# Kernel optimization log

Hardware: AMD Instinct MI355X
Metric: run time of the kernel (lower is better)

## Reference

```python
import jax, jax.numpy as jnp
import numpy as np

NH, NL, NP, GA = 8, 4, 4, 8  # num_heads, num_levels, num_points, grid_align_num
SHAPES = np.array([[128, 128], [64, 64], [32, 32], [16, 16]], dtype=np.int64)  # (W, H) per level


def _grid_sample(img, grid):
    """F.grid_sample bilinear, padding_mode='zeros', align_corners=False.
    img: [N,C,H,W], grid: [N,Hg,Wg,2] in [-1,1] (x,y). Returns [N,C,Hg,Wg]."""
    N, C, H, W = img.shape
    x = (grid[..., 0] + 1.0) * (W * 0.5) - 0.5
    y = (grid[..., 1] + 1.0) * (H * 0.5) - 0.5
    x0 = jnp.floor(x)
    y0 = jnp.floor(y)
    wx = (x - x0)[:, None]  # [N,1,Hg,Wg]
    wy = (y - y0)[:, None]
    x0i = x0.astype(jnp.int32)
    y0i = y0.astype(jnp.int32)
    img_flat = img.reshape(N, C, H * W)
    Hg, Wg = grid.shape[1], grid.shape[2]

    def tap(ix, iy):
        valid = (ix >= 0) & (ix < W) & (iy >= 0) & (iy < H)
        lin = jnp.clip(iy, 0, H - 1) * W + jnp.clip(ix, 0, W - 1)
        v = jnp.take_along_axis(img_flat, lin.reshape(N, 1, Hg * Wg), axis=2)
        return v.reshape(N, C, Hg, Wg) * valid[:, None].astype(img.dtype)

    v00 = tap(x0i, y0i)
    v01 = tap(x0i + 1, y0i)
    v10 = tap(x0i, y0i + 1)
    v11 = tap(x0i + 1, y0i + 1)
    return (v00 * (1 - wx) * (1 - wy) + v01 * wx * (1 - wy)
            + v10 * (1 - wx) * wy + v11 * wx * wy)


def setup_inputs() -> dict:
    key = jax.random.key(0)
    ks = jax.random.split(key, 6)
    bs, nq, E = 2, 16384, 256
    total = int((SHAPES[:, 0] * SHAPES[:, 1]).sum())  # 21760
    query = jax.random.normal(ks[0], (bs, nq, E), jnp.float32)
    value = jax.random.normal(ks[1], (bs, total, NH, E // NH), jnp.float32)
    reference_points = jax.random.uniform(ks[2], (bs, nq, 1, NL * 2), jnp.float32)
    W_off = jax.random.normal(ks[3], (NH * NL * NP * 2, E), jnp.float32) * 0.01
    # structured offset bias per init_weights (directional rays, radius ~ point index)
    thetas = jnp.arange(NH, dtype=jnp.float32) * (2.0 * np.pi / NH)
    gi = jnp.stack([jnp.cos(thetas), jnp.sin(thetas)], -1)  # [NH,2]
    gi = gi / jnp.max(jnp.abs(gi), axis=-1, keepdims=True)
    gi = jnp.tile(gi[:, None, None, :], (1, NL, NP, 1))
    gi = gi * jnp.arange(1, NP + 1, dtype=jnp.float32)[None, None, :, None]
    b_off = gi.reshape(-1)
    W_attn = jax.random.normal(ks[4], (NH * NL * NP, E), jnp.float32) * 0.01
    b_attn = jax.random.normal(ks[5], (NH * NL * NP,), jnp.float32) * 0.01
    return {"query": query, "value": value, "reference_points": reference_points,
            "W_off": W_off, "b_off": b_off, "W_attn": W_attn, "b_attn": b_attn,
            "spatial_shapes": np.asarray(SHAPES)}


def reference(query, value, reference_points, W_off, b_off, W_attn, b_attn, spatial_shapes):
    bs, nq, E = query.shape
    d = E // NH
    shapes = np.asarray(spatial_shapes)  # static [L,2] (W,H)

    # sampling offsets and locations (non-deploy path)
    off = (query @ W_off.T + b_off).reshape(bs, nq, NH, NL * NP * 2)
    ref = jnp.tile(reference_points, (1, 1, NH, NP)).reshape(bs, nq, NH, NL * NP * 2)
    # offset_normalizer: (1/spatial_shapes).repeat(1, NP).flatten() -> layout (l, p, xy)
    norm = jnp.asarray(np.tile(1.0 / shapes.astype(np.float32), (1, NP)).reshape(-1))
    loc = (ref + off * norm) * 2.0 - 1.0  # [bs, nq, NH, NL*NP*2]

    # attention weights: softmax over levels*points, regrouped to (L, G, P) layout
    attn = jax.nn.softmax((query @ W_attn.T + b_attn).reshape(bs, nq, NH, NL * NP), axis=-1)
    attn = (attn.reshape(bs, nq // GA, GA, NH, NL, NP)
            .transpose(0, 3, 1, 4, 2, 5)
            .reshape(bs * NH, 1, nq // GA, NL * GA * NP))

    grids = loc.reshape(bs, nq, NH, NL, NP, 2)
    outs = []
    start = 0
    for lvl in range(NL):
        W_, H_ = int(shapes[lvl, 0]), int(shapes[lvl, 1])
        n = H_ * W_
        v = value[:, start:start + n].transpose(0, 2, 3, 1).reshape(bs * NH, d, H_, W_)
        start += n
        g = grids[:, :, :, lvl].transpose(0, 2, 1, 3, 4).reshape(bs * NH, nq // GA, GA * NP, 2)
        outs.append(_grid_sample(v, g))  # [bs*NH, d, nq//GA, GA*NP]
    samp = jnp.concatenate(outs, axis=-1) * attn  # [bs*NH, d, nq//GA, NL*GA*NP]
    # reduce_sum linear with fixed 0/1 weight == sum over levels and points per group slot
    out = samp.reshape(bs * NH, d, nq // GA, NL, GA, NP).sum(axis=(3, 5))
    return out.reshape(bs, NH * d, nq)
```

## Files before the change

kernel.cpp:

```cpp
#include <hip/hip_runtime.h>
#include <hip/hip_bf16.h>


typedef __attribute__((ext_vector_type(4))) float    float4v;
typedef __attribute__((ext_vector_type(8))) _Float16 half8;
typedef __attribute__((ext_vector_type(4))) _Float16 half4;
typedef __attribute__((ext_vector_type(2))) _Float16 half2v;

#define NQ    16384
#define NTOK  21760
#define LREC  48

#define GEMM_BLOCKS 768
#define CONV_BLOCKS 10880

union H8 { half8 v; half2v p[4]; };

#define LDSTR 88
__global__ __launch_bounds__(256) void fused_kernel(
    const float* __restrict__ qf,
    const float* __restrict__ Woff, const float* __restrict__ Wattn,
    const float* __restrict__ boff, const float* __restrict__ battn,
    const float* __restrict__ val,
    _Float16* __restrict__ lh, _Float16* __restrict__ vh) {
  const int tid = threadIdx.x;

  if (blockIdx.x >= GEMM_BLOCKS) {
    int i = (blockIdx.x - GEMM_BLOCKS) * 256 + tid;
    float4v v = ((const float4v*)val)[i];
    half4 o;
    o[0] = (_Float16)v[0]; o[1] = (_Float16)v[1];
    o[2] = (_Float16)v[2]; o[3] = (_Float16)v[3];
    ((half4*)vh)[i] = o;
    return;
  }

  __shared__ _Float16 As[128 * LDSTR];
  __shared__ _Float16 Bs[128 * LDSTR];

  const int lane = tid & 63;
  const int wv   = tid >> 6;
  const int wm   = wv >> 1, wn = wv & 1;
  const int quad = lane >> 4;
  const int r    = lane & 15;
  const int blockM = (blockIdx.x & 255) * 128;
  const int n0     = (blockIdx.x >> 8) * 128;

  float4v acc[4][4];
#pragma unroll
  for (int i = 0; i < 4; ++i)
#pragma unroll
    for (int j = 0; j < 4; ++j) acc[i][j] = (float4v){0.f, 0.f, 0.f, 0.f};

  for (int kc = 0; kc < 4; ++kc) {
    const int k0 = kc * 64;
    if (kc) __syncthreads();
#pragma unroll
    for (int it = 0; it < 8; ++it) {
      int idx = it * 256 + tid;
      int row = idx >> 4, k4 = idx & 15;
      float4v v = *(const float4v*)(qf + (size_t)(blockM + row) * 256 + k0 + k4 * 4);
      half4 o;
      o[0] = (_Float16)v[0]; o[1] = (_Float16)v[1];
      o[2] = (_Float16)v[2]; o[3] = (_Float16)v[3];
      *(half4*)&As[row * LDSTR + k4 * 4] = o;
    }
#pragma unroll
    for (int it = 0; it < 8; ++it) {
      int idx = it * 256 + tid;
      int row = idx >> 4, k4 = idx & 15;
      int n = n0 + row;
      const float* src = (n < 256) ? (Woff + (size_t)n * 256)
                                   : (Wattn + (size_t)(n - 256) * 256);
      float4v v = *(const float4v*)(src + k0 + k4 * 4);
      half4 o;
      o[0] = (_Float16)v[0]; o[1] = (_Float16)v[1];
      o[2] = (_Float16)v[2]; o[3] = (_Float16)v[3];
      *(half4*)&Bs[row * LDSTR + k4 * 4] = o;
    }
    __syncthreads();

#pragma unroll
    for (int kf = 0; kf < 2; ++kf) {
      const int ko = kf * 32 + quad * 8;
      half8 af[4], bf[4];
#pragma unroll
      for (int mi = 0; mi < 4; ++mi)
        af[mi] = *(const half8*)&As[(wm * 64 + mi * 16 + r) * LDSTR + ko];
#pragma unroll
      for (int ni = 0; ni < 4; ++ni)
        bf[ni] = *(const half8*)&Bs[(wn * 64 + ni * 16 + r) * LDSTR + ko];
#pragma unroll
      for (int mi = 0; mi < 4; ++mi)
#pragma unroll
        for (int ni = 0; ni < 4; ++ni)
          acc[mi][ni] = __builtin_amdgcn_mfma_f32_16x16x32_f16(af[mi], bf[ni], acc[mi][ni], 0, 0, 0);
    }
  }

#pragma unroll
  for (int mi = 0; mi < 4; ++mi) {
    const int mb = blockM + wm * 64 + mi * 16 + quad * 4;
#pragma unroll
    for (int ni = 0; ni < 4; ++ni) {
      const int n = n0 + wn * 64 + ni * 16 + r;
      const float bias = (n < 256) ? boff[n] : battn[n - 256];
      const int h    = (n < 256) ? (n >> 5) : ((n - 256) >> 4);
      const int slot = (n < 256) ? (n & 31) : (32 + ((n - 256) & 15));
#pragma unroll
      for (int reg = 0; reg < 4; ++reg) {
        const int bq = mb + reg;
        const int b = bq >> 14, q = bq & 16383;
        lh[((size_t)(b * 8 + h) * NQ + q) * LREC + slot] =
            (_Float16)(acc[mi][ni][reg] + bias);
      }
    }
  }
}

__global__ __launch_bounds__(256) void sample_kernel(
    const _Float16* __restrict__ vh, const float* __restrict__ refp,
    const _Float16* __restrict__ lh, float* __restrict__ out) {
  const int bid   = blockIdx.x;
  const int xcd   = bid & 7;
  const int local = bid >> 3;
  const int hb    = xcd * 2 + (local >> 8);
  const int qt    = local & 255;
  const int h     = hb & 7;
  const int b     = hb >> 3;
  const int tid = threadIdx.x;
  const int c4 = tid & 3;
  const int qi = tid >> 2;
  const int q  = qt * 64 + qi;
  const size_t bq = (size_t)b * NQ + q;
  const _Float16* rec = lh + ((size_t)hb * NQ + q) * LREC;

  float offf[32];
#pragma unroll
  for (int i = 0; i < 4; ++i) {
    half8 oh = *(const half8*)(rec + i * 8);
#pragma unroll
    for (int j = 0; j < 8; ++j) offf[i * 8 + j] = (float)oh[j];
  }
  float al[16];
#pragma unroll
  for (int i = 0; i < 2; ++i) {
    half8 ah = *(const half8*)(rec + 32 + i * 8);
#pragma unroll
    for (int j = 0; j < 8; ++j) al[i * 8 + j] = (float)ah[j];
  }
  float mx = -1e30f;
#pragma unroll
  for (int i = 0; i < 16; ++i) mx = fmaxf(mx, al[i]);
  float ssum = 0.f;
#pragma unroll
  for (int i = 0; i < 16; ++i) {
    float e = __expf(al[i] - mx);
    al[i] = e;
    ssum += e;
  }
  const float inv = 1.0f / ssum;

  float4v rp0 = *(const float4v*)(refp + bq * 8);
  float4v rp1 = *(const float4v*)(refp + bq * 8 + 4);
  const float rpx[4] = {rp0[0], rp0[2], rp1[0], rp1[2]};
  const float rpy[4] = {rp0[1], rp0[3], rp1[1], rp1[3]};

  const _Float16* vb = vh + (size_t)b * NTOK * 256 + h * 32 + c4 * 8;
  float4v acc0 = (float4v){0.f, 0.f, 0.f, 0.f};
  float4v acc1 = (float4v){0.f, 0.f, 0.f, 0.f};

  const int base[4] = {0, 16384, 20480, 21504};

#pragma unroll
  for (int l = 0; l < 4; ++l) {
    const int   W  = 128 >> l;
    const float fW = (float)W;
    const _Float16* vlev = vb + (size_t)base[l] * 256;
    half2v accl[4];
#pragma unroll
    for (int j = 0; j < 4; ++j) accl[j] = (half2v){(_Float16)0, (_Float16)0};
#pragma unroll
    for (int p = 0; p < 4; ++p) {
      const float a  = al[l * 4 + p] * inv;
      const float ox = offf[l * 8 + p * 2];
      const float oy = offf[l * 8 + p * 2 + 1];
      const float x = rpx[p] * fW + ox - 0.5f;
      const float y = rpy[p] * fW + oy - 0.5f;
      const float xf = floorf(x), yf = floorf(y);
      const float fx = x - xf, fy = y - yf;
      const int ix = (int)xf, iy = (int)yf;
      const int ix0 = min(max(ix, 0), W - 1);
      const int ix1 = min(max(ix + 1, 0), W - 1);
      const int iy0 = min(max(iy, 0), W - 1);
      const int iy1 = min(max(iy + 1, 0), W - 1);
      const float wx0 = ((unsigned)ix       < (unsigned)W) ? 1.f - fx : 0.f;
      const float wx1 = ((unsigned)(ix + 1) < (unsigned)W) ? fx       : 0.f;
      const float wy0 = ((unsigned)iy       < (unsigned)W) ? 1.f - fy : 0.f;
      const float wy1 = ((unsigned)(iy + 1) < (unsigned)W) ? fy       : 0.f;
      const _Float16 w00 = (_Float16)(a * wx0 * wy0);
      const _Float16 w01 = (_Float16)(a * wx1 * wy0);
      const _Float16 w10 = (_Float16)(a * wx0 * wy1);
      const _Float16 w11 = (_Float16)(a * wx1 * wy1);
      const half2v h00 = (half2v){w00, w00};
      const half2v h01 = (half2v){w01, w01};
      const half2v h10 = (half2v){w10, w10};
      const half2v h11 = (half2v){w11, w11};
      const _Float16* r0 = vlev + (size_t)(iy0 * W) * 256;
      const _Float16* r1 = vlev + (size_t)(iy1 * W) * 256;
      H8 t00, t01, t10, t11;
      t00.v = *(const half8*)(r0 + ix0 * 256);
      t01.v = *(const half8*)(r0 + ix1 * 256);
      t10.v = *(const half8*)(r1 + ix0 * 256);
      t11.v = *(const half8*)(r1 + ix1 * 256);
#pragma unroll
      for (int j = 0; j < 4; ++j) {
        accl[j] += h00 * t00.p[j] + h01 * t01.p[j]
                 + h10 * t10.p[j] + h11 * t11.p[j];
      }
    }
    acc0[0] += (float)accl[0][0]; acc0[1] += (float)accl[0][1];
    acc0[2] += (float)accl[1][0]; acc0[3] += (float)accl[1][1];
    acc1[0] += (float)accl[2][0]; acc1[1] += (float)accl[2][1];
    acc1[2] += (float)accl[3][0]; acc1[3] += (float)accl[3][1];
  }

  __shared__ float sm[32][65];
#pragma unroll
  for (int j = 0; j < 4; ++j) {
    sm[c4 * 8 + j][qi]     = acc0[j];
    sm[c4 * 8 + 4 + j][qi] = acc1[j];
  }
  __syncthreads();
  const size_t obase = ((size_t)b * 256 + h * 32) * NQ + qt * 64;
#pragma unroll
  for (int i = 0; i < 8; ++i) {
    const int idx = i * 256 + tid;
    const int c = idx >> 6, qq = idx & 63;
    out[obase + (size_t)c * NQ + qq] = sm[c][qq];
  }
}

extern "C" void kernel_launch(void* const* d_in, const int* in_sizes, int n_in,
                              void* d_out, int out_size, void* d_ws, size_t ws_size,
                              hipStream_t stream) {
  const float* query = (const float*)d_in[0];
  const float* value = (const float*)d_in[1];
  const float* refp  = (const float*)d_in[2];
  const float* Woff  = (const float*)d_in[3];
  const float* boff  = (const float*)d_in[4];
  const float* Wattn = (const float*)d_in[5];
  const float* battn = (const float*)d_in[6];
  float* out = (float*)d_out;

  char* ws = (char*)d_ws;
  _Float16* vh = (_Float16*)ws;
  _Float16* lh = (_Float16*)(ws + 22282240);

  fused_kernel<<<GEMM_BLOCKS + CONV_BLOCKS, 256, 0, stream>>>(
      query, Woff, Wattn, boff, battn, value, lh, vh);
  sample_kernel<<<4096, 256, 0, stream>>>(vh, refp, lh, out);
}
```

Baseline: 221.7 us.

## Assign one query per thread with all 32 channels in sample kernel

Reworks the sampling kernel so each thread handles one query across all 32 head channels instead of four threads sharing a query with 8 channels each. Offsets, softmax and bilinear weights are computed once per query rather than replicated four times, and the corner gathers become four contiguous 64-byte reads per thread. In exchange, each thread carries far more registers (32 fp32 accumulators, 16 half2 accumulators, 16 half8 loads), which may cut occupancy, and the block size and grid are halved.

```diff
diff --git a/kernel.cpp b/kernel.cpp
--- a/kernel.cpp
+++ b/kernel.cpp
@@ -118,30 +118,25 @@
   }
 }
 
-__global__ __launch_bounds__(256) void sample_kernel(
+__global__ __launch_bounds__(128) void sample_kernel(
     const _Float16* __restrict__ vh, const float* __restrict__ refp,
     const _Float16* __restrict__ lh, float* __restrict__ out) {
   const int bid   = blockIdx.x;
   const int xcd   = bid & 7;
   const int local = bid >> 3;
-  const int hb    = xcd * 2 + (local >> 8);
-  const int qt    = local & 255;
+  const int hb    = xcd * 2 + (local >> 7);
+  const int qt    = local & 127;
   const int h     = hb & 7;
   const int b     = hb >> 3;
-  const int tid = threadIdx.x;
-  const int c4 = tid & 3;
-  const int qi = tid >> 2;
-  const int q  = qt * 64 + qi;
+  const int tid   = threadIdx.x;
+  const int q     = qt * 128 + tid;
   const size_t bq = (size_t)b * NQ + q;
   const _Float16* rec = lh + ((size_t)hb * NQ + q) * LREC;
 
-  float offf[32];
-#pragma unroll
-  for (int i = 0; i < 4; ++i) {
-    half8 oh = *(const half8*)(rec + i * 8);
-#pragma unroll
-    for (int j = 0; j < 8; ++j) offf[i * 8 + j] = (float)oh[j];
-  }
+  half8 oh[4];
+#pragma unroll
+  for (int i = 0; i < 4; ++i) oh[i] = *(const half8*)(rec + i * 8);
+
   float al[16];
 #pragma unroll
   for (int i = 0; i < 2; ++i) {
@@ -160,15 +155,19 @@
     ssum += e;
   }
   const float inv = 1.0f / ssum;
+#pragma unroll
+  for (int i = 0; i < 16; ++i) al[i] *= inv;
 
   float4v rp0 = *(const float4v*)(refp + bq * 8);
   float4v rp1 = *(const float4v*)(refp + bq * 8 + 4);
   const float rpx[4] = {rp0[0], rp0[2], rp1[0], rp1[2]};
   const float rpy[4] = {rp0[1], rp0[3], rp1[1], rp1[3]};
 
-  const _Float16* vb = vh + (size_t)b * NTOK * 256 + h * 32 + c4 * 8;
-  float4v acc0 = (float4v){0.f, 0.f, 0.f, 0.f};
-  float4v acc1 = (float4v){0.f, 0.f, 0.f, 0.f};
+  const _Float16* vb = vh + (size_t)b * NTOK * 256 + h * 32;
+
+  float accf[32];
+#pragma unroll
+  for (int i = 0; i < 32; ++i) accf[i] = 0.f;
 
   const int base[4] = {0, 16384, 20480, 21504};
 
@@ -177,14 +176,14 @@
     const int   W  = 128 >> l;
     const float fW = (float)W;
     const _Float16* vlev = vb + (size_t)base[l] * 256;
-    half2v accl[4];
-#pragma unroll
-    for (int j = 0; j < 4; ++j) accl[j] = (half2v){(_Float16)0, (_Float16)0};
+    half2v accl[16];
+#pragma unroll
+    for (int j = 0; j < 16; ++j) accl[j] = (half2v){(_Float16)0, (_Float16)0};
 #pragma unroll
     for (int p = 0; p < 4; ++p) {
-      const float a  = al[l * 4 + p] * inv;
-      const float ox = offf[l * 8 + p * 2];
-      const float oy = offf[l * 8 + p * 2 + 1];
+      const float a  = al[l * 4 + p];
+      const float ox = (float)oh[l][p * 2];
+      const float oy = (float)oh[l][p * 2 + 1];
       const float x = rpx[p] * fW + ox - 0.5f;
       const float y = rpy[p] * fW + oy - 0.5f;
       const float xf = floorf(x), yf = floorf(y);
@@ -206,37 +205,43 @@
       const half2v h01 = (half2v){w01, w01};
       const half2v h10 = (half2v){w10, w10};
       const half2v h11 = (half2v){w11, w11};
-      const _Float16* r0 = vlev + (size_t)(iy0 * W) * 256;
-      const _Float16* r1 = vlev + (size_t)(iy1 * W) * 256;
-      H8 t00, t01, t10, t11;
-      t00.v = *(const half8*)(r0 + ix0 * 256);
-      t01.v = *(const half8*)(r0 + ix1 * 256);
-      t10.v = *(const half8*)(r1 + ix0 * 256);
-      t11.v = *(const half8*)(r1 + ix1 * 256);
+      const _Float16* p00 = vlev + (size_t)(iy0 * W + ix0) * 256;
+      const _Float16* p01 = vlev + (size_t)(iy0 * W + ix1) * 256;
+      const _Float16* p10 = vlev + (size_t)(iy1 * W + ix0) * 256;
+      const _Float16* p11 = vlev + (size_t)(iy1 * W + ix1) * 256;
+      H8 t00[4], t01[4], t10[4], t11[4];
 #pragma unroll
       for (int j = 0; j < 4; ++j) {
-        accl[j] += h00 * t00.p[j] + h01 * t01.p[j]
-                 + h10 * t10.p[j] + h11 * t11.p[j];
+        t00[j].v = *(const half8*)(p00 + j * 8);
+        t01[j].v = *(const half8*)(p01 + j * 8);
+        t10[j].v = *(const half8*)(p10 + j * 8);
+        t11[j].v = *(const half8*)(p11 + j * 8);
       }
-    }
-    acc0[0] += (float)accl[0][0]; acc0[1] += (float)accl[0][1];
-    acc0[2] += (float)accl[1][0]; acc0[3] += (float)accl[1][1];
-    acc1[0] += (float)accl[2][0]; acc1[1] += (float)accl[2][1];
-    acc1[2] += (float)accl[3][0]; acc1[3] += (float)accl[3][1];
-  }
-
-  __shared__ float sm[32][65];
-#pragma unroll
-  for (int j = 0; j < 4; ++j) {
-    sm[c4 * 8 + j][qi]     = acc0[j];
-    sm[c4 * 8 + 4 + j][qi] = acc1[j];
-  }
+#pragma unroll
+      for (int j = 0; j < 4; ++j)
+#pragma unroll
+        for (int k = 0; k < 4; ++k)
+          accl[j * 4 + k] += h00 * t00[j].p[k] + h01 * t01[j].p[k]
+                           + h10 * t10[j].p[k] + h11 * t11[j].p[k];
+    }
+#pragma unroll
+    for (int j = 0; j < 4; ++j)
+#pragma unroll
+      for (int k = 0; k < 4; ++k) {
+        accf[j * 8 + k * 2]     += (float)accl[j * 4 + k][0];
+        accf[j * 8 + k * 2 + 1] += (float)accl[j * 4 + k][1];
+      }
+  }
+
+  __shared__ float sm[32][129];
+#pragma unroll
+  for (int c = 0; c < 32; ++c) sm[c][tid] = accf[c];
   __syncthreads();
-  const size_t obase = ((size_t)b * 256 + h * 32) * NQ + qt * 64;
-#pragma unroll
-  for (int i = 0; i < 8; ++i) {
-    const int idx = i * 256 + tid;
-    const int c = idx >> 6, qq = idx & 63;
+  const size_t obase = ((size_t)b * 256 + h * 32) * NQ + qt * 128;
+#pragma unroll
+  for (int i = 0; i < 32; ++i) {
+    const int idx = i * 128 + tid;
+    const int c = idx >> 7, qq = idx & 127;
     out[obase + (size_t)c * NQ + qq] = sm[c][qq];
   }
 }
@@ -259,5 +264,5 @@
 
   fused_kernel<<<GEMM_BLOCKS + CONV_BLOCKS, 256, 0, stream>>>(
       query, Woff, Wattn, boff, battn, value, lh, vh);
-  sample_kernel<<<4096, 256, 0, stream>>>(vh, refp, lh, out);
+  sample_kernel<<<2048, 128, 0, stream>>>(vh, refp, lh, out);
 }
```

Measured after the change: 370.5 us. +67.1%, slower.

## Split sampling across levels per thread and reduce level partials in shared memory

Applied to the files above, without the earlier changes.

Each thread in the sample kernel now handles a single feature level instead of looping over all four, so a block covers 16 queries instead of 64 and the grid grows fourfold. Per-level partial sums go to shared memory and are summed across levels before the coalesced store. The aim is more parallelism and memory-level concurrency for the latency-bound gather loads, plus fewer registers per thread. In exchange, the softmax max and sum and the reference-point loads are repeated by each of the four level threads, and there is extra shared-memory traffic.

```diff
diff --git a/kernel.cpp b/kernel.cpp
--- a/kernel.cpp
+++ b/kernel.cpp
@@ -124,24 +124,19 @@
   const int bid   = blockIdx.x;
   const int xcd   = bid & 7;
   const int local = bid >> 3;
-  const int hb    = xcd * 2 + (local >> 8);
-  const int qt    = local & 255;
+  const int hb    = xcd * 2 + (local >> 10);
+  const int qt    = local & 1023;
   const int h     = hb & 7;
   const int b     = hb >> 3;
   const int tid = threadIdx.x;
   const int c4 = tid & 3;
-  const int qi = tid >> 2;
-  const int q  = qt * 64 + qi;
+  const int l  = (tid >> 2) & 3;
+  const int qi = tid >> 4;
+  const int q  = qt * 16 + qi;
   const size_t bq = (size_t)b * NQ + q;
   const _Float16* rec = lh + ((size_t)hb * NQ + q) * LREC;
 
-  float offf[32];
-#pragma unroll
-  for (int i = 0; i < 4; ++i) {
-    half8 oh = *(const half8*)(rec + i * 8);
-#pragma unroll
-    for (int j = 0; j < 8; ++j) offf[i * 8 + j] = (float)oh[j];
-  }
+  const half8 oh = *(const half8*)(rec + l * 8);
   float al[16];
 #pragma unroll
   for (int i = 0; i < 2; ++i) {
@@ -149,16 +144,14 @@
 #pragma unroll
     for (int j = 0; j < 8; ++j) al[i * 8 + j] = (float)ah[j];
   }
+  const half4 ownl = *(const half4*)(rec + 32 + l * 4);
+
   float mx = -1e30f;
 #pragma unroll
   for (int i = 0; i < 16; ++i) mx = fmaxf(mx, al[i]);
   float ssum = 0.f;
 #pragma unroll
-  for (int i = 0; i < 16; ++i) {
-    float e = __expf(al[i] - mx);
-    al[i] = e;
-    ssum += e;
-  }
+  for (int i = 0; i < 16; ++i) ssum += __expf(al[i] - mx);
   const float inv = 1.0f / ssum;
 
   float4v rp0 = *(const float4v*)(refp + bq * 8);
@@ -166,78 +159,77 @@
   const float rpx[4] = {rp0[0], rp0[2], rp1[0], rp1[2]};
   const float rpy[4] = {rp0[1], rp0[3], rp1[1], rp1[3]};
 
-  const _Float16* vb = vh + (size_t)b * NTOK * 256 + h * 32 + c4 * 8;
-  float4v acc0 = (float4v){0.f, 0.f, 0.f, 0.f};
-  float4v acc1 = (float4v){0.f, 0.f, 0.f, 0.f};
-
-  const int base[4] = {0, 16384, 20480, 21504};
-
-#pragma unroll
-  for (int l = 0; l < 4; ++l) {
-    const int   W  = 128 >> l;
-    const float fW = (float)W;
-    const _Float16* vlev = vb + (size_t)base[l] * 256;
-    half2v accl[4];
-#pragma unroll
-    for (int j = 0; j < 4; ++j) accl[j] = (half2v){(_Float16)0, (_Float16)0};
-#pragma unroll
-    for (int p = 0; p < 4; ++p) {
-      const float a  = al[l * 4 + p] * inv;
-      const float ox = offf[l * 8 + p * 2];
-      const float oy = offf[l * 8 + p * 2 + 1];
-      const float x = rpx[p] * fW + ox - 0.5f;
-      const float y = rpy[p] * fW + oy - 0.5f;
-      const float xf = floorf(x), yf = floorf(y);
-      const float fx = x - xf, fy = y - yf;
-      const int ix = (int)xf, iy = (int)yf;
-      const int ix0 = min(max(ix, 0), W - 1);
-      const int ix1 = min(max(ix + 1, 0), W - 1);
-      const int iy0 = min(max(iy, 0), W - 1);
-      const int iy1 = min(max(iy + 1, 0), W - 1);
-      const float wx0 = ((unsigned)ix       < (unsigned)W) ? 1.f - fx : 0.f;
-      const float wx1 = ((unsigned)(ix + 1) < (unsigned)W) ? fx       : 0.f;
-      const float wy0 = ((unsigned)iy       < (unsigned)W) ? 1.f - fy : 0.f;
-      const float wy1 = ((unsigned)(iy + 1) < (unsigned)W) ? fy       : 0.f;
-      const _Float16 w00 = (_Float16)(a * wx0 * wy0);
-      const _Float16 w01 = (_Float16)(a * wx1 * wy0);
-      const _Float16 w10 = (_Float16)(a * wx0 * wy1);
-      const _Float16 w11 = (_Float16)(a * wx1 * wy1);
-      const half2v h00 = (half2v){w00, w00};
-      const half2v h01 = (half2v){w01, w01};
-      const half2v h10 = (half2v){w10, w10};
-      const half2v h11 = (half2v){w11, w11};
-      const _Float16* r0 = vlev + (size_t)(iy0 * W) * 256;
-      const _Float16* r1 = vlev + (size_t)(iy1 * W) * 256;
-      H8 t00, t01, t10, t11;
-      t00.v = *(const half8*)(r0 + ix0 * 256);
-      t01.v = *(const half8*)(r0 + ix1 * 256);
-      t10.v = *(const half8*)(r1 + ix0 * 256);
-      t11.v = *(const half8*)(r1 + ix1 * 256);
-#pragma unroll
-      for (int j = 0; j < 4; ++j) {
-        accl[j] += h00 * t00.p[j] + h01 * t01.p[j]
-                 + h10 * t10.p[j] + h11 * t11.p[j];
-      }
-    }
-    acc0[0] += (float)accl[0][0]; acc0[1] += (float)accl[0][1];
-    acc0[2] += (float)accl[1][0]; acc0[3] += (float)accl[1][1];
-    acc1[0] += (float)accl[2][0]; acc1[1] += (float)accl[2][1];
-    acc1[2] += (float)accl[3][0]; acc1[3] += (float)accl[3][1];
-  }
-
-  __shared__ float sm[32][65];
+  const int   W    = 128 >> l;
+  const float fW   = (float)W;
+  const int   base = (l == 0) ? 0 : (l == 1) ? 16384 : (l == 2) ? 20480 : 21504;
+  const _Float16* vlev = vh + (size_t)b * NTOK * 256 + h * 32 + c4 * 8
+                            + (size_t)base * 256;
+
+  half2v accl0 = (half2v){(_Float16)0, (_Float16)0};
+  half2v accl1 = (half2v){(_Float16)0, (_Float16)0};
+  half2v accl2 = (half2v){(_Float16)0, (_Float16)0};
+  half2v accl3 = (half2v){(_Float16)0, (_Float16)0};
+
+#pragma unroll
+  for (int p = 0; p < 4; ++p) {
+    const float a  = __expf((float)ownl[p] - mx) * inv;
+    const float ox = (float)oh[p * 2];
+    const float oy = (float)oh[p * 2 + 1];
+    const float x = rpx[p] * fW + ox - 0.5f;
+    const float y = rpy[p] * fW + oy - 0.5f;
+    const float xf = floorf(x), yf = floorf(y);
+    const float fx = x - xf, fy = y - yf;
+    const int ix = (int)xf, iy = (int)yf;
+    const int ix0 = min(max(ix, 0), W - 1);
+    const int ix1 = min(max(ix + 1, 0), W - 1);
+    const int iy0 = min(max(iy, 0), W - 1);
+    const int iy1 = min(max(iy + 1, 0), W - 1);
+    const float wx0 = ((unsigned)ix       < (unsigned)W) ? 1.f - fx : 0.f;
+    const float wx1 = ((unsigned)(ix + 1) < (unsigned)W) ? fx       : 0.f;
+    const float wy0 = ((unsigned)iy       < (unsigned)W) ? 1.f - fy : 0.f;
+    const float wy1 = ((unsigned)(iy + 1) < (unsigned)W) ? fy       : 0.f;
+    const _Float16 w00 = (_Float16)(a * wx0 * wy0);
+    const _Float16 w01 = (_Float16)(a * wx1 * wy0);
+    const _Float16 w10 = (_Float16)(a * wx0 * wy1);
+    const _Float16 w11 = (_Float16)(a * wx1 * wy1);
+    const half2v h00 = (half2v){w00, w00};
+    const half2v h01 = (half2v){w01, w01};
+    const half2v h10 = (half2v){w10, w10};
+    const half2v h11 = (half2v){w11, w11};
+    const _Float16* r0 = vlev + (size_t)(iy0 * W) * 256;
+    const _Float16* r1 = vlev + (size_t)(iy1 * W) * 256;
+    H8 t00, t01, t10, t11;
+    t00.v = *(const half8*)(r0 + ix0 * 256);
+    t01.v = *(const half8*)(r0 + ix1 * 256);
+    t10.v = *(const half8*)(r1 + ix0 * 256);
+    t11.v = *(const half8*)(r1 + ix1 * 256);
+    accl0 += h00 * t00.p[0] + h01 * t01.p[0] + h10 * t10.p[0] + h11 * t11.p[0];
+    accl1 += h00 * t00.p[1] + h01 * t01.p[1] + h10 * t10.p[1] + h11 * t11.p[1];
+    accl2 += h00 * t00.p[2] + h01 * t01.p[2] + h10 * t10.p[2] + h11 * t11.p[2];
+    accl3 += h00 * t00.p[3] + h01 * t01.p[3] + h10 * t10.p[3] + h11 * t11.p[3];
+  }
+
+  float acc0[4], acc1[4];
+  acc0[0] = (float)accl0[0]; acc0[1] = (float)accl0[1];
+  acc0[2] = (float)accl1[0]; acc0[3] = (float)accl1[1];
+  acc1[0] = (float)accl2[0]; acc1[1] = (float)accl2[1];
+  acc1[2] = (float)accl3[0]; acc1[3] = (float)accl3[1];
+
+  __shared__ float sm[4][16][33];
 #pragma unroll
   for (int j = 0; j < 4; ++j) {
-    sm[c4 * 8 + j][qi]     = acc0[j];
-    sm[c4 * 8 + 4 + j][qi] = acc1[j];
+    sm[l][qi][c4 * 8 + j]     = acc0[j];
+    sm[l][qi][c4 * 8 + 4 + j] = acc1[j];
   }
   __syncthreads();
-  const size_t obase = ((size_t)b * 256 + h * 32) * NQ + qt * 64;
-#pragma unroll
-  for (int i = 0; i < 8; ++i) {
+  const size_t obase = ((size_t)b * 256 + h * 32) * NQ + qt * 16;
+#pragma unroll
+  for (int i = 0; i < 2; ++i) {
     const int idx = i * 256 + tid;
-    const int c = idx >> 6, qq = idx & 63;
-    out[obase + (size_t)c * NQ + qq] = sm[c][qq];
+    const int c  = idx >> 4;
+    const int ql = idx & 15;
+    const float v = ((sm[0][ql][c] + sm[1][ql][c]) + sm[2][ql][c]) + sm[3][ql][c];
+    out[obase + (size_t)c * NQ + ql] = v;
   }
 }
 
@@ -259,5 +251,5 @@
 
   fused_kernel<<<GEMM_BLOCKS + CONV_BLOCKS, 256, 0, stream>>>(
       query, Woff, Wattn, boff, battn, value, lh, vh);
-  sample_kernel<<<4096, 256, 0, stream>>>(vh, refp, lh, out);
+  sample_kernel<<<16384, 256, 0, stream>>>(vh, refp, lh, out);
 }
```

New measurement: 215.9 us. -2.6%, faster.
